# Optimization experiments

Hardware: AMD Instinct MI355X
Metric: run time of the kernel (lower is better)

## Reference

```python
import jax, jax.numpy as jnp
import numpy as np


def setup_inputs() -> dict:
    key = jax.random.key(0)
    ks = jax.random.split(key, 7)
    N, D, K = 500000, 128, 32
    return {
        "x": jax.random.normal(ks[0], (N, D), dtype=jnp.float32),
        "h_e": jax.random.normal(ks[1], (N, D), dtype=jnp.float32),
        "bond_n": jax.random.uniform(ks[2], (K, N), dtype=jnp.float32),
        "W_i_w": jax.random.normal(ks[3], (D, 2 * D), dtype=jnp.float32) * 0.05,
        "W_i_b": jax.random.normal(ks[4], (D,), dtype=jnp.float32) * 0.05,
        "W_m_w": jax.random.normal(ks[5], (D, D), dtype=jnp.float32) * 0.05,
        "W_m_b": jax.random.normal(ks[6], (D,), dtype=jnp.float32) * 0.05,
    }


def reference(x, h_e, bond_n, W_i_w, W_i_b, W_m_w, W_m_b):
    # h_n = relu(W_i([x ; h_e]))  -> [N, D]
    h_n = jax.nn.relu(jnp.concatenate([x, h_e], axis=1) @ W_i_w.T + W_i_b)
    # m = sum_k sum_n bond_n[k,n] * h_n[n,:]  -> [D]
    # (equivalent to torch: (bond_n[...,None] * h_n).sum(1).sum(0),
    #  but expressed as a contraction to avoid the [K,N,D] intermediate)
    m = jnp.einsum('kn,nd->d', bond_n, h_n)
    # h = relu(h_n + W_m(m))  -> [N, D] via broadcast of the [D] message
    h = jax.nn.relu(h_n + (m @ W_m_w.T + W_m_b))
    return h
```

## Files before the change

kernel.cpp:

```cpp
#include <hip/hip_runtime.h>
#include <stdint.h>
#include <stddef.h>

#define N_ROWS 500000
#define DDIM   128
#define K2     256
#define KBOND  32
#define TILE   32
#define NTL    (N_ROWS / TILE)
#define NBLK   768
#define MR_BLKS 12
#define P2_BLOCKS 2048

typedef float  f32x4  __attribute__((ext_vector_type(4)));
typedef __bf16 bf16x8 __attribute__((ext_vector_type(8)));
typedef __bf16 bf16x4 __attribute__((ext_vector_type(4)));

__device__ __bf16 g_wbf[DDIM * K2];
__device__ float  g_s[N_ROWS];
__device__ float  g_partials[NBLK * DDIM];
__device__ float  g_p2[MR_BLKS * DDIM];
__device__ float  g_msg[DDIM];
__device__ __bf16 g_hn[(size_t)N_ROWS * DDIM];

#define BARSEQ() do {                                   \
    __builtin_amdgcn_sched_barrier(0);                  \
    asm volatile("s_waitcnt lgkmcnt(0)");               \
    __builtin_amdgcn_s_barrier();                       \
    __builtin_amdgcn_sched_barrier(0);                  \
  } while (0)

__global__ void k_prep(const float* __restrict__ w) {
  int t = blockIdx.x * blockDim.x + threadIdx.x;
  if (t < DDIM * K2) g_wbf[t] = (__bf16)w[t];
}

__global__ __launch_bounds__(256)
void k_s(const float* __restrict__ bond) {
  int n = blockIdx.x * 256 + threadIdx.x;
  if (n >= N_ROWS) return;
  float a = 0.f, b = 0.f;
  #pragma unroll
  for (int k = 0; k < KBOND; k += 2) {
    a += bond[(size_t)k * N_ROWS + n];
    b += bond[(size_t)(k + 1) * N_ROWS + n];
  }
  g_s[n] = a + b;
}

__global__ __launch_bounds__(512, 6)
void k_pass1(const float* __restrict__ x, const float* __restrict__ he,
             const float* __restrict__ bias)
{
  __shared__ __align__(16) unsigned char a_lds[2][TILE * 512];

  const int tid  = threadIdx.x;
  const int w    = tid >> 6;
  const int lane = tid & 63;
  const int l15  = lane & 15;
  const int g    = lane >> 4;

  bf16x8 wfrag[8];
  #pragma unroll
  for (int ks = 0; ks < 8; ++ks)
    wfrag[ks] = *(const bf16x8*)(g_wbf + (size_t)(16 * w + l15) * K2 + 32 * ks + 8 * g);

  const int d0 = 16 * w + 4 * g;
  const f32x4 bv = *(const f32x4*)(bias + d0);

  const int sr = tid >> 4;
  const int sc = tid & 15;
  const unsigned swz   = (unsigned)((sr & 15) << 4);
  const unsigned wo_x  = (unsigned)(sr * 512) + ((16u * sc) ^ swz);
  const unsigned wo_he = (unsigned)(sr * 512) + 256u + ((16u * sc) ^ swz);
  const unsigned rsw   = (unsigned)(l15 << 4);

  f32x4 macc = (f32x4)(0.f);

  int t = blockIdx.x;

  {
    const float* xr = x  + (size_t)(t * TILE + sr) * DDIM + 8 * sc;
    const float* hr = he + (size_t)(t * TILE + sr) * DDIM + 8 * sc;
    f32x4 xa = *(const f32x4*)xr, xb = *(const f32x4*)(xr + 4);
    f32x4 ha = *(const f32x4*)hr, hb = *(const f32x4*)(hr + 4);
    bf16x8 bx, bh;
    #pragma unroll
    for (int i = 0; i < 4; ++i) {
      bx[i] = (__bf16)xa[i]; bx[4 + i] = (__bf16)xb[i];
      bh[i] = (__bf16)ha[i]; bh[4 + i] = (__bf16)hb[i];
    }
    *(bf16x8*)(&a_lds[0][wo_x])  = bx;
    *(bf16x8*)(&a_lds[0][wo_he]) = bh;
  }
  float s0 = g_s[t * TILE + l15];
  float s1 = g_s[t * TILE + 16 + l15];
  BARSEQ();

  int cur = 0;
  while (true) {
    const int  tn  = t + NBLK;
    const bool has = tn < NTL;
    const int  tl  = has ? tn : t;

    const float* xr = x  + (size_t)(tl * TILE + sr) * DDIM + 8 * sc;
    const float* hr = he + (size_t)(tl * TILE + sr) * DDIM + 8 * sc;
    f32x4 xa = *(const f32x4*)xr, xb = *(const f32x4*)(xr + 4);
    f32x4 ha = *(const f32x4*)hr, hb = *(const f32x4*)(hr + 4);
    float s0n = g_s[tl * TILE + l15];
    float s1n = g_s[tl * TILE + 16 + l15];
    __builtin_amdgcn_sched_barrier(0);

    f32x4 acc0 = (f32x4)(0.f), acc1 = (f32x4)(0.f);
    const unsigned char* base = &a_lds[cur][0];
    #pragma unroll
    for (int ks = 0; ks < 8; ++ks) {
      const unsigned o = (unsigned)(64 * ks + 16 * g);
      bf16x8 b0 = *(const bf16x8*)(base + l15 * 512        + (o ^ rsw));
      bf16x8 b1 = *(const bf16x8*)(base + (16 + l15) * 512 + (o ^ rsw));
      acc0 = __builtin_amdgcn_mfma_f32_16x16x32_bf16(wfrag[ks], b0, acc0, 0, 0, 0);
      acc1 = __builtin_amdgcn_mfma_f32_16x16x32_bf16(wfrag[ks], b1, acc1, 0, 0, 0);
    }

    {
      const int rb = t * TILE;
      f32x4 h0, h1;
      #pragma unroll
      for (int i = 0; i < 4; ++i) {
        float a = acc0[i] + bv[i]; h0[i] = a > 0.f ? a : 0.f;
        float b = acc1[i] + bv[i]; h1[i] = b > 0.f ? b : 0.f;
      }
      #pragma unroll
      for (int i = 0; i < 4; ++i) macc[i] += s0 * h0[i] + s1 * h1[i];
      bf16x4 hb0, hb1;
      #pragma unroll
      for (int i = 0; i < 4; ++i) { hb0[i] = (__bf16)h0[i]; hb1[i] = (__bf16)h1[i]; }
      *(bf16x4*)(g_hn + (size_t)(rb + l15) * DDIM + d0)      = hb0;
      *(bf16x4*)(g_hn + (size_t)(rb + 16 + l15) * DDIM + d0) = hb1;
    }
    __builtin_amdgcn_sched_barrier(0);

    {
      bf16x8 bx, bh;
      #pragma unroll
      for (int i = 0; i < 4; ++i) {
        bx[i] = (__bf16)xa[i]; bx[4 + i] = (__bf16)xb[i];
        bh[i] = (__bf16)ha[i]; bh[4 + i] = (__bf16)hb[i];
      }
      *(bf16x8*)(&a_lds[cur ^ 1][wo_x])  = bx;
      *(bf16x8*)(&a_lds[cur ^ 1][wo_he]) = bh;
    }
    BARSEQ();

    if (!has) break;
    t = tn; cur ^= 1; s0 = s0n; s1 = s1n;
  }

  #pragma unroll
  for (int off = 1; off <= 8; off <<= 1) {
    #pragma unroll
    for (int i = 0; i < 4; ++i) macc[i] += __shfl_xor(macc[i], off, 64);
  }
  if (l15 == 0)
    *(f32x4*)(&g_partials[(size_t)blockIdx.x * DDIM + d0]) = macc;
}

__global__ void k_mr() {
  const int d    = threadIdx.x & 127;
  const int half = threadIdx.x >> 7;
  const int r0   = blockIdx.x * 64;
  float acc = 0.f;
  for (int r = r0 + half; r < r0 + 64; r += 2)
    acc += g_partials[(size_t)r * DDIM + d];
  __shared__ float sp[DDIM];
  if (half == 0) sp[d] = acc;
  __syncthreads();
  if (half == 1) g_p2[blockIdx.x * DDIM + d] = sp[d] + acc;
}

__global__ void k_msg(const float* __restrict__ wm, const float* __restrict__ bm) {
  __shared__ float ms[DDIM];
  const int d = threadIdx.x;
  float s = 0.f;
  #pragma unroll
  for (int c = 0; c < MR_BLKS; ++c) s += g_p2[c * DDIM + d];
  ms[d] = s;
  __syncthreads();
  float acc = bm[d];
  #pragma unroll 8
  for (int j = 0; j < DDIM; ++j) acc += ms[j] * wm[(size_t)d * DDIM + j];
  g_msg[d] = acc;
}

__global__ __launch_bounds__(256)
void k_pass2(float* __restrict__ out)
{
  __shared__ float ms[DDIM];
  if (threadIdx.x < DDIM) ms[threadIdx.x] = g_msg[threadIdx.x];
  __syncthreads();
  const size_t total = (size_t)N_ROWS * DDIM / 8;
  for (size_t c = (size_t)blockIdx.x * blockDim.x + threadIdx.x; c < total;
       c += (size_t)gridDim.x * blockDim.x) {
    const size_t base = c * 8;
    const int col0 = (int)(base & (DDIM - 1));
    bf16x8 hv = *(const bf16x8*)(g_hn + base);
    f32x4 o0, o1;
    #pragma unroll
    for (int i = 0; i < 4; ++i) {
      float a = (float)hv[i]     + ms[col0 + i];
      float b = (float)hv[4 + i] + ms[col0 + 4 + i];
      o0[i] = a > 0.f ? a : 0.f;
      o1[i] = b > 0.f ? b : 0.f;
    }
    *(f32x4*)(out + base)     = o0;
    *(f32x4*)(out + base + 4) = o1;
  }
}

extern "C" void kernel_launch(void* const* d_in, const int* in_sizes, int n_in,
                              void* d_out, int out_size, void* d_ws, size_t ws_size,
                              hipStream_t stream) {
  const float* x    = (const float*)d_in[0];
  const float* he   = (const float*)d_in[1];
  const float* bond = (const float*)d_in[2];
  const float* wi   = (const float*)d_in[3];
  const float* bi   = (const float*)d_in[4];
  const float* wm   = (const float*)d_in[5];
  const float* bm   = (const float*)d_in[6];
  float* out = (float*)d_out;
  (void)d_ws; (void)ws_size;

  k_prep<<<(DDIM * K2 + 255) / 256, 256, 0, stream>>>(wi);
  k_s<<<(N_ROWS + 255) / 256, 256, 0, stream>>>(bond);
  k_pass1<<<NBLK, 512, 0, stream>>>(x, he, bi);
  k_mr<<<MR_BLKS, 256, 0, stream>>>();
  k_msg<<<1, 128, 0, stream>>>(wm, bm);
  k_pass2<<<P2_BLOCKS, 256, 0, stream>>>(out);
}
```

Measured before the change: 298.6 us.

## Stage fp32 inputs via direct global-to-LDS loads with 16-row tiles

Pass 1 now copies x and h_e rows straight into LDS as fp32 with global_load_lds, using an XOR swizzle. The conversion to bf16 moves to after the LDS read, so the register staging and the separate LDS write step go away. The tile shrinks from 32 to 16 rows to fit the larger fp32 LDS buffers, which halves the MFMA work per iteration and doubles the number of loop iterations and barriers. The barrier now waits on vmcnt(1), which relies on a particular ordering of outstanding loads (the g_s load and the bf16 hn store) and may be fragile.

```diff
diff --git a/kernel.cpp b/kernel.cpp
--- a/kernel.cpp
+++ b/kernel.cpp
@@ -6,7 +6,7 @@
 #define DDIM   128
 #define K2     256
 #define KBOND  32
-#define TILE   32
+#define TILE   16
 #define NTL    (N_ROWS / TILE)
 #define NBLK   768
 #define MR_BLKS 12
@@ -23,12 +23,11 @@
 __device__ float  g_msg[DDIM];
 __device__ __bf16 g_hn[(size_t)N_ROWS * DDIM];
 
-#define BARSEQ() do {                                   \
-    __builtin_amdgcn_sched_barrier(0);                  \
-    asm volatile("s_waitcnt lgkmcnt(0)");               \
-    __builtin_amdgcn_s_barrier();                       \
-    __builtin_amdgcn_sched_barrier(0);                  \
-  } while (0)
+static __device__ __forceinline__ void gload16(const float* g, float* l) {
+  __builtin_amdgcn_global_load_lds(
+      (const __attribute__((address_space(1))) void*)g,
+      (__attribute__((address_space(3))) void*)l, 16, 0, 0);
+}
 
 __global__ void k_prep(const float* __restrict__ w) {
   int t = blockIdx.x * blockDim.x + threadIdx.x;
@@ -52,7 +51,7 @@
 void k_pass1(const float* __restrict__ x, const float* __restrict__ he,
              const float* __restrict__ bias)
 {
-  __shared__ __align__(16) unsigned char a_lds[2][TILE * 512];
+  __shared__ __align__(1024) float a_lds[2][TILE * K2];
 
   const int tid  = threadIdx.x;
   const int w    = tid >> 6;
@@ -68,34 +67,28 @@
   const int d0 = 16 * w + 4 * g;
   const f32x4 bv = *(const f32x4*)(bias + d0);
 
-  const int sr = tid >> 4;
-  const int sc = tid & 15;
-  const unsigned swz   = (unsigned)((sr & 15) << 4);
-  const unsigned wo_x  = (unsigned)(sr * 512) + ((16u * sc) ^ swz);
-  const unsigned wo_he = (unsigned)(sr * 512) + 256u + ((16u * sc) ^ swz);
-  const unsigned rsw   = (unsigned)(l15 << 4);
+  int   soff[2];
+  const float* sarr[2];
+  #pragma unroll
+  for (int j = 0; j < 2; ++j) {
+    const int r  = 2 * w + j;
+    const int sl = lane ^ (r & 7);
+    sarr[j] = (sl < 32) ? x : he;
+    soff[j] = (sl < 32) ? 4 * sl : 4 * sl - 128;
+  }
 
   f32x4 macc = (f32x4)(0.f);
-
   int t = blockIdx.x;
 
-  {
-    const float* xr = x  + (size_t)(t * TILE + sr) * DDIM + 8 * sc;
-    const float* hr = he + (size_t)(t * TILE + sr) * DDIM + 8 * sc;
-    f32x4 xa = *(const f32x4*)xr, xb = *(const f32x4*)(xr + 4);
-    f32x4 ha = *(const f32x4*)hr, hb = *(const f32x4*)(hr + 4);
-    bf16x8 bx, bh;
-    #pragma unroll
-    for (int i = 0; i < 4; ++i) {
-      bx[i] = (__bf16)xa[i]; bx[4 + i] = (__bf16)xb[i];
-      bh[i] = (__bf16)ha[i]; bh[4 + i] = (__bf16)hb[i];
-    }
-    *(bf16x8*)(&a_lds[0][wo_x])  = bx;
-    *(bf16x8*)(&a_lds[0][wo_he]) = bh;
-  }
+  #pragma unroll
+  for (int j = 0; j < 2; ++j)
+    gload16(sarr[j] + (size_t)(t * TILE + 2 * w + j) * DDIM + soff[j],
+            &a_lds[0][(2 * w + j) * K2]);
   float s0 = g_s[t * TILE + l15];
-  float s1 = g_s[t * TILE + 16 + l15];
-  BARSEQ();
+  __builtin_amdgcn_sched_barrier(0);
+  asm volatile("s_waitcnt vmcnt(0)");
+  __builtin_amdgcn_s_barrier();
+  __builtin_amdgcn_sched_barrier(0);
 
   int cur = 0;
   while (true) {
@@ -103,57 +96,50 @@
     const bool has = tn < NTL;
     const int  tl  = has ? tn : t;
 
-    const float* xr = x  + (size_t)(tl * TILE + sr) * DDIM + 8 * sc;
-    const float* hr = he + (size_t)(tl * TILE + sr) * DDIM + 8 * sc;
-    f32x4 xa = *(const f32x4*)xr, xb = *(const f32x4*)(xr + 4);
-    f32x4 ha = *(const f32x4*)hr, hb = *(const f32x4*)(hr + 4);
+    #pragma unroll
+    for (int j = 0; j < 2; ++j)
+      gload16(sarr[j] + (size_t)(tl * TILE + 2 * w + j) * DDIM + soff[j],
+              &a_lds[cur ^ 1][(2 * w + j) * K2]);
     float s0n = g_s[tl * TILE + l15];
-    float s1n = g_s[tl * TILE + 16 + l15];
     __builtin_amdgcn_sched_barrier(0);
 
-    f32x4 acc0 = (f32x4)(0.f), acc1 = (f32x4)(0.f);
-    const unsigned char* base = &a_lds[cur][0];
+    f32x4 acc = (f32x4)(0.f);
+    const char* base = (const char*)&a_lds[cur][0];
+    const unsigned rowb = (unsigned)(l15 * 1024);
+    const unsigned p    = (unsigned)(l15 & 7);
     #pragma unroll
     for (int ks = 0; ks < 8; ++ks) {
-      const unsigned o = (unsigned)(64 * ks + 16 * g);
-      bf16x8 b0 = *(const bf16x8*)(base + l15 * 512        + (o ^ rsw));
-      bf16x8 b1 = *(const bf16x8*)(base + (16 + l15) * 512 + (o ^ rsw));
-      acc0 = __builtin_amdgcn_mfma_f32_16x16x32_bf16(wfrag[ks], b0, acc0, 0, 0, 0);
-      acc1 = __builtin_amdgcn_mfma_f32_16x16x32_bf16(wfrag[ks], b1, acc1, 0, 0, 0);
+      const unsigned sA = (unsigned)(8 * ks + 2 * g);
+      const unsigned aA = rowb + 16u * (sA ^ p);
+      f32x4 A = *(const f32x4*)(base + aA);
+      f32x4 B = *(const f32x4*)(base + (aA ^ 16u));
+      bf16x8 b;
+      #pragma unroll
+      for (int i = 0; i < 4; ++i) { b[i] = (__bf16)A[i]; b[4 + i] = (__bf16)B[i]; }
+      acc = __builtin_amdgcn_mfma_f32_16x16x32_bf16(wfrag[ks], b, acc, 0, 0, 0);
     }
 
     {
-      const int rb = t * TILE;
-      f32x4 h0, h1;
+      f32x4 h;
       #pragma unroll
       for (int i = 0; i < 4; ++i) {
-        float a = acc0[i] + bv[i]; h0[i] = a > 0.f ? a : 0.f;
-        float b = acc1[i] + bv[i]; h1[i] = b > 0.f ? b : 0.f;
+        float v = acc[i] + bv[i]; h[i] = v > 0.f ? v : 0.f;
       }
       #pragma unroll
-      for (int i = 0; i < 4; ++i) macc[i] += s0 * h0[i] + s1 * h1[i];
-      bf16x4 hb0, hb1;
-      #pragma unroll
-      for (int i = 0; i < 4; ++i) { hb0[i] = (__bf16)h0[i]; hb1[i] = (__bf16)h1[i]; }
-      *(bf16x4*)(g_hn + (size_t)(rb + l15) * DDIM + d0)      = hb0;
-      *(bf16x4*)(g_hn + (size_t)(rb + 16 + l15) * DDIM + d0) = hb1;
+      for (int i = 0; i < 4; ++i) macc[i] += s0 * h[i];
+      bf16x4 hb;
+      #pragma unroll
+      for (int i = 0; i < 4; ++i) hb[i] = (__bf16)h[i];
+      *(bf16x4*)(g_hn + (size_t)(t * TILE + l15) * DDIM + d0) = hb;
     }
+
     __builtin_amdgcn_sched_barrier(0);
-
-    {
-      bf16x8 bx, bh;
-      #pragma unroll
-      for (int i = 0; i < 4; ++i) {
-        bx[i] = (__bf16)xa[i]; bx[4 + i] = (__bf16)xb[i];
-        bh[i] = (__bf16)ha[i]; bh[4 + i] = (__bf16)hb[i];
-      }
-      *(bf16x8*)(&a_lds[cur ^ 1][wo_x])  = bx;
-      *(bf16x8*)(&a_lds[cur ^ 1][wo_he]) = bh;
-    }
-    BARSEQ();
+    asm volatile("s_waitcnt vmcnt(1)");
+    __builtin_amdgcn_s_barrier();
+    __builtin_amdgcn_sched_barrier(0);
 
     if (!has) break;
-    t = tn; cur ^= 1; s0 = s0n; s1 = s1n;
+    t = tn; cur ^= 1; s0 = s0n;
   }
 
   #pragma unroll
```

New measurement: 281.2 us. -5.8%, faster.
